# Optimization experiments

Hardware: AMD Instinct MI355X
Metric: run time of the kernel (lower is better)

## Reference

```python
import jax, jax.numpy as jnp
import numpy as np

N = 65536        # number of encoding vectors (flattened tokens)
K = 1024         # num_embeddings (codebook size)
D = 128          # embedding_dim
BETA = 0.25


def setup_inputs() -> dict:
    key = jax.random.key(0)
    k_enc, k_cb = jax.random.split(key)
    encoding = jax.random.normal(k_enc, (N, D), dtype=jnp.float32)
    # nn.Embedding weight initialized uniform(-1/K, 1/K)
    codebook = jax.random.uniform(k_cb, (K, D), dtype=jnp.float32,
                                  minval=-1.0 / K, maxval=1.0 / K)
    return {"encoding": encoding, "codebook": codebook}


def reference(encoding, codebook):
    # Nearest codebook entry per row. argmin of L2 distance == argmin of
    # squared distance; expand ||e - w||^2 = ||e||^2 - 2 e.w + ||w||^2.
    # ||e||^2 is constant per row, so it does not affect the argmin.
    scores = (-2.0 * jnp.einsum('nd,kd->nk', encoding, codebook)
              + jnp.sum(codebook * codebook, axis=-1)[None, :])  # [N, K]
    quantized_index = jnp.argmin(scores, axis=-1)                # [N] int
    quantized_embedding = codebook[quantized_index]              # [N, D] gather == onehot @ W

    sg = jax.lax.stop_gradient
    commitment_loss = jnp.mean((sg(quantized_embedding) - encoding) ** 2)
    embedding_loss = jnp.mean((quantized_embedding - sg(encoding)) ** 2)
    vq_loss = commitment_loss * BETA + embedding_loss

    # straight-through estimator
    quantized_st = encoding + sg(quantized_embedding - encoding)

    quantized_index = quantized_index[:, None]  # match torch unsqueeze(1) -> [N, 1]
    return (quantized_index, quantized_st, vq_loss, embedding_loss, commitment_loss)
```

## Files before the change

kernel.cpp:

```cpp
#include <hip/hip_runtime.h>


#define NROWS 65536
#define KCB   1024
#define DIM   128
#define DV    32
#define MSE_DENOM 8388608.0f
#define MARGIN 3.0e-5f
#define MARGINS 0.030720f
#define FLAGCAP 16384
#define CSCALE   1024.0f
#define CDESCALE 0.0009765625f

#define WS_CNORM_F  256
#define WS_CN1024_F 1280
#define WS_LIST_B   12288
#define WS_PH_B     77824
#define WS_NEEDED   339968

typedef __attribute__((ext_vector_type(16))) float float16v;
typedef _Float16 half8 __attribute__((ext_vector_type(8)));
union U4H8 { uint4 u; half8 h; };
union F4A  { float4 v; float f[4]; };
union F16V { float16v v; float f[16]; };
union HU   { _Float16 f; unsigned short u; };

__device__ __forceinline__ float fmed3(float a, float b, float c) {
  return __builtin_amdgcn_fmed3f(a, b, c);
}

__global__ __launch_bounds__(256) void vq_prep_pack(const float* __restrict__ C,
                                                    float* __restrict__ wsf,
                                                    uint4* __restrict__ PH) {
  const int b = blockIdx.x;
  if (b < 64) {
    int g = b * 256 + threadIdx.x;
    int mt = g >> 9, s = (g >> 6) & 7, l = g & 63;
    int cw = mt * 32 + (l & 31);
    int k0 = s * 16 + (l >> 5) * 8;
    const float* src = C + (size_t)cw * DIM + k0;
    float4 x0 = *(const float4*)src;
    float4 x1 = *(const float4*)(src + 4);
    unsigned h[8];
    {
      float v[8] = {x0.x, x0.y, x0.z, x0.w, x1.x, x1.y, x1.z, x1.w};
#pragma unroll
      for (int j = 0; j < 8; ++j) { HU u; u.f = (_Float16)(CSCALE * v[j]); h[j] = u.u; }
    }
    PH[g] = make_uint4(h[0] | (h[1] << 16), h[2] | (h[3] << 16),
                       h[4] | (h[5] << 16), h[6] | (h[7] << 16));
  } else {
    int k = (b - 64) * 256 + threadIdx.x;
    if (k == 0) { wsf[0] = 0.0f; ((unsigned*)wsf)[1] = 0u; }
    const float4* c4 = (const float4*)C + (size_t)k * DV;
    float s = 0.f;
#pragma unroll 8
    for (int i = 0; i < DV; ++i) {
      float4 v = c4[i];
      s = fmaf(v.x, v.x, s); s = fmaf(v.y, v.y, s);
      s = fmaf(v.z, v.z, s); s = fmaf(v.w, v.w, s);
    }
    wsf[WS_CNORM_F + k]  = s;
    wsf[WS_CN1024_F + k] = s * CSCALE;
  }
}

__global__ __launch_bounds__(256, 2) void vq_main11(const float* __restrict__ E,
                                                    const float* __restrict__ C,
                                                    float* __restrict__ wsf,
                                                    float* __restrict__ out) {
  __shared__ int BI[128];

  const int tid  = threadIdx.x;
  const int w    = tid >> 6;
  const int l    = tid & 63;
  const int half = l >> 5;
  const int rr   = l & 31;
  const int row0 = blockIdx.x * 128;
  const int row  = row0 + w * 32 + rr;

  const uint4*  PHg = (const uint4*)((const char*)wsf + WS_PH_B);
  const float4* CNb = (const float4*)(wsf + WS_CN1024_F);

  half8 beh[8];
  float s2 = 0.f;
  const float* erow = E + (size_t)row * DIM + half * 8;
#pragma unroll
  for (int s = 0; s < 8; ++s) {
    float4 x0 = *(const float4*)(erow + s * 16);
    float4 x1 = *(const float4*)(erow + s * 16 + 4);
    float v[8] = {x0.x, x0.y, x0.z, x0.w, x1.x, x1.y, x1.z, x1.w};
#pragma unroll
    for (int j = 0; j < 8; ++j) {
      float y = v[j];
      s2 = fmaf(y, y, s2);
      beh[s][j] = (_Float16)(-2.f * y);
    }
  }

  float m1 = 3.0e38f, m2 = 3.0e38f;
  int   bi = 0;

#pragma unroll 4
  for (int tg = 0; tg < 32; ++tg) {
    const uint4* src = PHg + (size_t)tg * 512 + l;
    U4H8 h0, h1, h2, h3, h4, h5, h6, h7;
    h0.u = src[0];   h1.u = src[64];  h2.u = src[128]; h3.u = src[192];
    h4.u = src[256]; h5.u = src[320]; h6.u = src[384]; h7.u = src[448];

    const float4* cn = CNb + tg * 8 + half;
    F4A c0, c1, c2, c3;
    c0.v = cn[0]; c1.v = cn[2]; c2.v = cn[4]; c3.v = cn[6];

    F16V accA, accB;
    accA.f[0]  = c0.f[0]; accA.f[1]  = c0.f[1]; accA.f[2]  = c0.f[2]; accA.f[3]  = c0.f[3];
    accA.f[4]  = c1.f[0]; accA.f[5]  = c1.f[1]; accA.f[6]  = c1.f[2]; accA.f[7]  = c1.f[3];
    accA.f[8]  = c2.f[0]; accA.f[9]  = c2.f[1]; accA.f[10] = c2.f[2]; accA.f[11] = c2.f[3];
    accA.f[12] = c3.f[0]; accA.f[13] = c3.f[1]; accA.f[14] = c3.f[2]; accA.f[15] = c3.f[3];
    accB.v = (float16v){0,0,0,0,0,0,0,0,0,0,0,0,0,0,0,0};

    accA.v = __builtin_amdgcn_mfma_f32_32x32x16_f16(h0.h, beh[0], accA.v, 0, 0, 0);
    accB.v = __builtin_amdgcn_mfma_f32_32x32x16_f16(h1.h, beh[1], accB.v, 0, 0, 0);
    accA.v = __builtin_amdgcn_mfma_f32_32x32x16_f16(h2.h, beh[2], accA.v, 0, 0, 0);
    accB.v = __builtin_amdgcn_mfma_f32_32x32x16_f16(h3.h, beh[3], accB.v, 0, 0, 0);
    accA.v = __builtin_amdgcn_mfma_f32_32x32x16_f16(h4.h, beh[4], accA.v, 0, 0, 0);
    accB.v = __builtin_amdgcn_mfma_f32_32x32x16_f16(h5.h, beh[5], accB.v, 0, 0, 0);
    accA.v = __builtin_amdgcn_mfma_f32_32x32x16_f16(h6.h, beh[6], accA.v, 0, 0, 0);
    accB.v = __builtin_amdgcn_mfma_f32_32x32x16_f16(h7.h, beh[7], accB.v, 0, 0, 0);

    const int kb = tg * 32 + half * 4;
#pragma unroll
    for (int reg = 0; reg < 16; ++reg) {
      float sc = accA.f[reg] + accB.f[reg];
      bool nb_ = sc < m1;
      m2 = fmed3(sc, m1, m2);
      m1 = fminf(sc, m1);
      bi = nb_ ? (kb + (reg >> 2) * 8 + (reg & 3)) : bi;
    }
  }

  {
    float om1 = __shfl_xor(m1, 32, 64);
    float om2 = __shfl_xor(m2, 32, 64);
    int   obi = __shfl_xor(bi, 32, 64);
    float nsv = fminf(fminf(m2, om2), fmaxf(m1, om1));
    if (om1 < m1 || (om1 == m1 && obi < bi)) { m1 = om1; bi = obi; }
    m2 = nsv;
  }
  float en = s2 + __shfl_xor(s2, 32, 64);

  if (half == 0) {
    const int r = w * 32 + rr;
    out[row] = (float)bi;
    BI[r] = bi;
    if (m2 - m1 < MARGINS) {
      unsigned idx = atomicAdd((unsigned*)wsf + 1, 1u);
      if (idx < FLAGCAP) ((int*)((char*)wsf + WS_LIST_B))[idx] = row;
    }
    float term = fmaf(m1, CDESCALE, en);
#pragma unroll
    for (int off = 16; off > 0; off >>= 1) term += __shfl_down(term, off);
    if (rr == 0) atomicAdd(wsf, term);
  }
  __syncthreads();

  const float4* C4   = (const float4*)C;
  float4*       out4 = (float4*)out;
#pragma unroll
  for (int it = 0; it < 16; ++it) {
    int flat = it * 256 + tid;
    int r = flat >> 5, d4 = flat & 31;
    out4[(NROWS / 4) + (size_t)(row0 + r) * DV + d4] = C4[(size_t)BI[r] * DV + d4];
  }
}

__global__ __launch_bounds__(256) void vq_fix(const float* __restrict__ E,
                                              const float* __restrict__ C,
                                              float* __restrict__ wsf,
                                              float* __restrict__ out) {
  __shared__ float4 eL[4][32];
  __shared__ float  RV[4][4];
  __shared__ int    RI[4][4];
  __shared__ int    RESi[4];
  const int tid = threadIdx.x;
  const int wv  = tid >> 6;
  const int ln  = tid & 63;

  if (blockIdx.x == 0 && tid == 0) {
    float mse = wsf[0] / MSE_DENOM;
    out[NROWS + NROWS * DIM + 0] = 1.25f * mse;
    out[NROWS + NROWS * DIM + 1] = mse;
    out[NROWS + NROWS * DIM + 2] = mse;
  }

  const int* list = (const int*)((const char*)wsf + WS_LIST_B);
  int nf = (int)((const unsigned*)wsf)[1];
  if (nf > FLAGCAP) nf = FLAGCAP;
  const float4* E4 = (const float4*)E;
  const float4* C4 = (const float4*)C;
  const float*  cn = wsf + WS_CNORM_F;
  float4* out4 = (float4*)out;

  for (int g = blockIdx.x; g * 4 < nf; g += gridDim.x) {
    const int base = g * 4;
    if (tid < 128) {
      int r = tid >> 5, d4 = tid & 31;
      int R = (base + r < nf) ? list[base + r] : list[base];
      eL[r][d4] = E4[(size_t)R * DV + d4];
    }
    __syncthreads();
    float bv[4] = {3.0e38f, 3.0e38f, 3.0e38f, 3.0e38f};
    int   bi[4] = {0, 0, 0, 0};
#pragma unroll
    for (int j = 0; j < 4; ++j) {
      int k = j * 256 + tid;
      float d0 = 0.f, d1 = 0.f, d2 = 0.f, d3 = 0.f;
#pragma unroll 4
      for (int d4 = 0; d4 < 32; ++d4) {
        float4 c = C4[(size_t)k * DV + d4];
        float4 e0 = eL[0][d4], e1 = eL[1][d4], e2 = eL[2][d4], e3 = eL[3][d4];
        d0 = fmaf(c.x, e0.x, d0); d0 = fmaf(c.y, e0.y, d0);
        d0 = fmaf(c.z, e0.z, d0); d0 = fmaf(c.w, e0.w, d0);
        d1 = fmaf(c.x, e1.x, d1); d1 = fmaf(c.y, e1.y, d1);
        d1 = fmaf(c.z, e1.z, d1); d1 = fmaf(c.w, e1.w, d1);
        d2 = fmaf(c.x, e2.x, d2); d2 = fmaf(c.y, e2.y, d2);
        d2 = fmaf(c.z, e2.z, d2); d2 = fmaf(c.w, e2.w, d2);
        d3 = fmaf(c.x, e3.x, d3); d3 = fmaf(c.y, e3.y, d3);
        d3 = fmaf(c.z, e3.z, d3); d3 = fmaf(c.w, e3.w, d3);
      }
      float cnk = cn[k];
      float s0 = fmaf(-2.f, d0, cnk);
      float s1 = fmaf(-2.f, d1, cnk);
      float s2 = fmaf(-2.f, d2, cnk);
      float s3 = fmaf(-2.f, d3, cnk);
      if (s0 < bv[0] || (s0 == bv[0] && k < bi[0])) { bv[0] = s0; bi[0] = k; }
      if (s1 < bv[1] || (s1 == bv[1] && k < bi[1])) { bv[1] = s1; bi[1] = k; }
      if (s2 < bv[2] || (s2 == bv[2] && k < bi[2])) { bv[2] = s2; bi[2] = k; }
      if (s3 < bv[3] || (s3 == bv[3] && k < bi[3])) { bv[3] = s3; bi[3] = k; }
    }
#pragma unroll
    for (int off = 32; off > 0; off >>= 1) {
#pragma unroll
      for (int r = 0; r < 4; ++r) {
        float wv_ = __shfl_down(bv[r], off);
        int   ji  = __shfl_down(bi[r], off);
        if (wv_ < bv[r] || (wv_ == bv[r] && ji < bi[r])) { bv[r] = wv_; bi[r] = ji; }
      }
    }
    if (ln == 0) {
#pragma unroll
      for (int r = 0; r < 4; ++r) { RV[wv][r] = bv[r]; RI[wv][r] = bi[r]; }
    }
    __syncthreads();
    if (tid < 4) {
      float v = RV[0][tid]; int i = RI[0][tid];
#pragma unroll
      for (int q = 1; q < 4; ++q) {
        float vv = RV[q][tid]; int ii = RI[q][tid];
        if (vv < v || (vv == v && ii < i)) { v = vv; i = ii; }
      }
      RESi[tid] = i;
      if (base + tid < nf) out[list[base + tid]] = (float)i;
    }
    __syncthreads();
    if (tid < 128) {
      int r = tid >> 5, d4 = tid & 31;
      if (base + r < nf) {
        int R = list[base + r];
        out4[(NROWS / 4) + (size_t)R * DV + d4] = C4[(size_t)RESi[r] * DV + d4];
      }
    }
    __syncthreads();
  }
}

__global__ __launch_bounds__(256) void vq_prep_fb(const float* __restrict__ C,
                                                  float* __restrict__ ws) {
  int k = blockIdx.x * 256 + threadIdx.x;
  if (k == 0) ws[0] = 0.0f;
  const float4* c4 = (const float4*)C + (size_t)k * DV;
  float s = 0.f;
#pragma unroll 8
  for (int i = 0; i < DV; ++i) {
    float4 v = c4[i];
    s = fmaf(v.x, v.x, s); s = fmaf(v.y, v.y, s);
    s = fmaf(v.z, v.z, s); s = fmaf(v.w, v.w, s);
  }
  ws[64 + k] = s;
}

__global__ __launch_bounds__(256) void vq_main_fb(const float* __restrict__ E,
                                                  const float* __restrict__ C,
                                                  const float* __restrict__ cnorm,
                                                  float* __restrict__ out,
                                                  float* __restrict__ lossacc) {
  __shared__ float smem[16384];
  float4* EsV = (float4*)smem;
  float4* CsV = (float4*)(smem + 8192);
  const int tid  = threadIdx.x;
  const int row0 = blockIdx.x * 64;
#pragma unroll
  for (int i = 0; i < 8; ++i) {
    int flat = i * 256 + tid;
    int r = flat >> 5, d4 = flat & 31;
    EsV[r * 32 + (d4 ^ (r & 31))] = ((const float4*)E)[(size_t)(row0 + r) * DV + d4];
  }
  const int tx = tid & 15, ty = tid >> 4;
  int rbase[4], rmask[4];
#pragma unroll
  for (int i = 0; i < 4; ++i) { int r = i * 16 + ty; rbase[i] = r * 32; rmask[i] = r & 31; }
  float bestv[4]; int besti[4];
#pragma unroll
  for (int i = 0; i < 4; ++i) { bestv[i] = 3.0e38f; besti[i] = 0; }
  for (int ch = 0; ch < 16; ++ch) {
    const int k0 = ch * 64;
    __syncthreads();
#pragma unroll
    for (int i = 0; i < 8; ++i) {
      int flat = i * 256 + tid;
      int k = flat >> 5, d4 = flat & 31;
      CsV[k * 32 + (d4 ^ (k & 31))] = ((const float4*)C)[(size_t)(k0 + k) * DV + d4];
    }
    __syncthreads();
    float acc[4][4] = {};
#pragma unroll 8
    for (int d4 = 0; d4 < DV; ++d4) {
      float4 a[4], b[4];
#pragma unroll
      for (int i = 0; i < 4; ++i) a[i] = EsV[rbase[i] + (d4 ^ rmask[i])];
#pragma unroll
      for (int j = 0; j < 4; ++j) { int k = j * 16 + tx; b[j] = CsV[k * 32 + (d4 ^ (k & 31))]; }
#pragma unroll
      for (int i = 0; i < 4; ++i)
#pragma unroll
        for (int j = 0; j < 4; ++j) {
          acc[i][j] = fmaf(a[i].x, b[j].x, acc[i][j]);
          acc[i][j] = fmaf(a[i].y, b[j].y, acc[i][j]);
          acc[i][j] = fmaf(a[i].z, b[j].z, acc[i][j]);
          acc[i][j] = fmaf(a[i].w, b[j].w, acc[i][j]);
        }
    }
#pragma unroll
    for (int j = 0; j < 4; ++j) {
      int kg = k0 + j * 16 + tx;
      float cnv = cnorm[kg];
#pragma unroll
      for (int i = 0; i < 4; ++i) {
        float s = fmaf(-2.0f, acc[i][j], cnv);
        if (s < bestv[i] || (s == bestv[i] && kg < besti[i])) { bestv[i] = s; besti[i] = kg; }
      }
    }
  }
  float* Rv = smem + 8192;
  int*   Ri = (int*)(smem + 9216);
  int*   BIf = (int*)(smem + 10240);
  __syncthreads();
#pragma unroll
  for (int i = 0; i < 4; ++i) {
    int r = i * 16 + ty;
    Rv[r * 16 + tx] = bestv[i];
    Ri[r * 16 + tx] = besti[i];
  }
  __syncthreads();
  if (tid < 64) {
    const int r = tid;
    float bv = Rv[r * 16]; int bi = Ri[r * 16];
#pragma unroll
    for (int t = 1; t < 16; ++t) {
      float v = Rv[r * 16 + t]; int ii = Ri[r * 16 + t];
      if (v < bv || (v == bv && ii < bi)) { bv = v; bi = ii; }
    }
    float en = 0.f;
#pragma unroll 8
    for (int d4 = 0; d4 < DV; ++d4) {
      float4 v = EsV[r * 32 + (d4 ^ (r & 31))];
      en = fmaf(v.x, v.x, en); en = fmaf(v.y, v.y, en);
      en = fmaf(v.z, v.z, en); en = fmaf(v.w, v.w, en);
    }
    out[row0 + r] = (float)bi;
    BIf[r] = bi;
    float blocksum = en + bv;
#pragma unroll
    for (int off = 32; off > 0; off >>= 1) blocksum += __shfl_down(blocksum, off);
    if (tid == 0) atomicAdd(lossacc, blocksum);
  }
  __syncthreads();
  const float4* C4   = (const float4*)C;
  float4*       out4 = (float4*)out;
  for (int flat = tid; flat < 64 * DV; flat += 256) {
    int r = flat >> 5, d4 = flat & 31;
    out4[(NROWS / 4) + (size_t)(row0 + r) * DV + d4] = C4[(size_t)BIf[r] * DV + d4];
  }
}

__global__ void vq_final_fb(const float* __restrict__ ws, float* __restrict__ out) {
  if (threadIdx.x == 0 && blockIdx.x == 0) {
    float mse = ws[0] / MSE_DENOM;
    out[NROWS + NROWS * DIM + 0] = 1.25f * mse;
    out[NROWS + NROWS * DIM + 1] = mse;
    out[NROWS + NROWS * DIM + 2] = mse;
  }
}

extern "C" void kernel_launch(void* const* d_in, const int* in_sizes, int n_in,
                              void* d_out, int out_size, void* d_ws, size_t ws_size,
                              hipStream_t stream) {
  const float* E = (const float*)d_in[0];
  const float* C = (const float*)d_in[1];
  float* out = (float*)d_out;
  float* wsf = (float*)d_ws;

  if (ws_size >= (size_t)WS_NEEDED) {
    uint4* PH = (uint4*)((char*)d_ws + WS_PH_B);
    vq_prep_pack<<<68, 256, 0, stream>>>(C, wsf, PH);
    vq_main11<<<NROWS / 128, 256, 0, stream>>>(E, C, wsf, out);
    vq_fix<<<512, 256, 0, stream>>>(E, C, wsf, out);
  } else {
    vq_prep_fb<<<4, 256, 0, stream>>>(C, wsf);
    vq_main_fb<<<NROWS / 64, 256, 0, stream>>>(E, C, wsf + 64, out, wsf);
    vq_final_fb<<<1, 64, 0, stream>>>(wsf, out);
  }
}
```

Before: 165.2 us.

## Split codebook across waves per 32-row block and merge top-2 via LDS

Each block now handles 32 rows instead of 128, and its four waves each scan a quarter of the codebook (8 tiles) for the same rows rather than all 32 tiles for separate rows. Per-wave best/second-best scores and indices are merged through shared memory before writing outputs and flagging near-ties. Occupancy is raised (launch bounds 5) and the two accumulators are collapsed into a single chained MFMA accumulator to cut registers. This trades a longer dependent MFMA chain, an extra barrier and 4x more blocks, each redundantly loading and converting the E rows in every wave, for shorter per-wave loops and more waves in flight.

```diff
diff --git a/kernel.cpp b/kernel.cpp
--- a/kernel.cpp
+++ b/kernel.cpp
@@ -65,19 +65,22 @@
   }
 }
 
-__global__ __launch_bounds__(256, 2) void vq_main11(const float* __restrict__ E,
+__global__ __launch_bounds__(256, 5) void vq_main12(const float* __restrict__ E,
                                                     const float* __restrict__ C,
                                                     float* __restrict__ wsf,
                                                     float* __restrict__ out) {
-  __shared__ int BI[128];
+  __shared__ float XM1[4][32];
+  __shared__ float XM2[4][32];
+  __shared__ int   XBI[4][32];
+  __shared__ int   BI[32];
 
   const int tid  = threadIdx.x;
   const int w    = tid >> 6;
   const int l    = tid & 63;
   const int half = l >> 5;
   const int rr   = l & 31;
-  const int row0 = blockIdx.x * 128;
-  const int row  = row0 + w * 32 + rr;
+  const int row0 = blockIdx.x * 32;
+  const int row  = row0 + rr;
 
   const uint4*  PHg = (const uint4*)((const char*)wsf + WS_PH_B);
   const float4* CNb = (const float4*)(wsf + WS_CN1024_F);
@@ -101,37 +104,41 @@
   float m1 = 3.0e38f, m2 = 3.0e38f;
   int   bi = 0;
 
-#pragma unroll 4
-  for (int tg = 0; tg < 32; ++tg) {
+#pragma unroll 2
+  for (int t = 0; t < 8; ++t) {
+    const int tg = w * 8 + t;
     const uint4* src = PHg + (size_t)tg * 512 + l;
-    U4H8 h0, h1, h2, h3, h4, h5, h6, h7;
-    h0.u = src[0];   h1.u = src[64];  h2.u = src[128]; h3.u = src[192];
-    h4.u = src[256]; h5.u = src[320]; h6.u = src[384]; h7.u = src[448];
 
     const float4* cn = CNb + tg * 8 + half;
     F4A c0, c1, c2, c3;
     c0.v = cn[0]; c1.v = cn[2]; c2.v = cn[4]; c3.v = cn[6];
-
-    F16V accA, accB;
-    accA.f[0]  = c0.f[0]; accA.f[1]  = c0.f[1]; accA.f[2]  = c0.f[2]; accA.f[3]  = c0.f[3];
-    accA.f[4]  = c1.f[0]; accA.f[5]  = c1.f[1]; accA.f[6]  = c1.f[2]; accA.f[7]  = c1.f[3];
-    accA.f[8]  = c2.f[0]; accA.f[9]  = c2.f[1]; accA.f[10] = c2.f[2]; accA.f[11] = c2.f[3];
-    accA.f[12] = c3.f[0]; accA.f[13] = c3.f[1]; accA.f[14] = c3.f[2]; accA.f[15] = c3.f[3];
-    accB.v = (float16v){0,0,0,0,0,0,0,0,0,0,0,0,0,0,0,0};
-
-    accA.v = __builtin_amdgcn_mfma_f32_32x32x16_f16(h0.h, beh[0], accA.v, 0, 0, 0);
-    accB.v = __builtin_amdgcn_mfma_f32_32x32x16_f16(h1.h, beh[1], accB.v, 0, 0, 0);
-    accA.v = __builtin_amdgcn_mfma_f32_32x32x16_f16(h2.h, beh[2], accA.v, 0, 0, 0);
-    accB.v = __builtin_amdgcn_mfma_f32_32x32x16_f16(h3.h, beh[3], accB.v, 0, 0, 0);
-    accA.v = __builtin_amdgcn_mfma_f32_32x32x16_f16(h4.h, beh[4], accA.v, 0, 0, 0);
-    accB.v = __builtin_amdgcn_mfma_f32_32x32x16_f16(h5.h, beh[5], accB.v, 0, 0, 0);
-    accA.v = __builtin_amdgcn_mfma_f32_32x32x16_f16(h6.h, beh[6], accA.v, 0, 0, 0);
-    accB.v = __builtin_amdgcn_mfma_f32_32x32x16_f16(h7.h, beh[7], accB.v, 0, 0, 0);
+    F16V acc;
+    acc.f[0]  = c0.f[0]; acc.f[1]  = c0.f[1]; acc.f[2]  = c0.f[2]; acc.f[3]  = c0.f[3];
+    acc.f[4]  = c1.f[0]; acc.f[5]  = c1.f[1]; acc.f[6]  = c1.f[2]; acc.f[7]  = c1.f[3];
+    acc.f[8]  = c2.f[0]; acc.f[9]  = c2.f[1]; acc.f[10] = c2.f[2]; acc.f[11] = c2.f[3];
+    acc.f[12] = c3.f[0]; acc.f[13] = c3.f[1]; acc.f[14] = c3.f[2]; acc.f[15] = c3.f[3];
+
+    {
+      U4H8 h0, h1, h2, h3;
+      h0.u = src[0];   h1.u = src[64];  h2.u = src[128]; h3.u = src[192];
+      acc.v = __builtin_amdgcn_mfma_f32_32x32x16_f16(h0.h, beh[0], acc.v, 0, 0, 0);
+      acc.v = __builtin_amdgcn_mfma_f32_32x32x16_f16(h1.h, beh[1], acc.v, 0, 0, 0);
+      acc.v = __builtin_amdgcn_mfma_f32_32x32x16_f16(h2.h, beh[2], acc.v, 0, 0, 0);
+      acc.v = __builtin_amdgcn_mfma_f32_32x32x16_f16(h3.h, beh[3], acc.v, 0, 0, 0);
+    }
+    {
+      U4H8 h4, h5, h6, h7;
+      h4.u = src[256]; h5.u = src[320]; h6.u = src[384]; h7.u = src[448];
+      acc.v = __builtin_amdgcn_mfma_f32_32x32x16_f16(h4.h, beh[4], acc.v, 0, 0, 0);
+      acc.v = __builtin_amdgcn_mfma_f32_32x32x16_f16(h5.h, beh[5], acc.v, 0, 0, 0);
+      acc.v = __builtin_amdgcn_mfma_f32_32x32x16_f16(h6.h, beh[6], acc.v, 0, 0, 0);
+      acc.v = __builtin_amdgcn_mfma_f32_32x32x16_f16(h7.h, beh[7], acc.v, 0, 0, 0);
+    }
 
     const int kb = tg * 32 + half * 4;
 #pragma unroll
     for (int reg = 0; reg < 16; ++reg) {
-      float sc = accA.f[reg] + accB.f[reg];
+      float sc = acc.f[reg];
       bool nb_ = sc < m1;
       m2 = fmed3(sc, m1, m2);
       m1 = fminf(sc, m1);
@@ -149,15 +156,26 @@
   }
   float en = s2 + __shfl_xor(s2, 32, 64);
 
-  if (half == 0) {
-    const int r = w * 32 + rr;
-    out[row] = (float)bi;
-    BI[r] = bi;
-    if (m2 - m1 < MARGINS) {
+  if (half == 0) { XM1[w][rr] = m1; XM2[w][rr] = m2; XBI[w][rr] = bi; }
+  __syncthreads();
+
+  if (w == 0 && half == 0) {
+    float b1 = XM1[0][rr], b2 = XM2[0][rr];
+    int   bb = XBI[0][rr];
+#pragma unroll
+    for (int q = 1; q < 4; ++q) {
+      float x1 = XM1[q][rr], x2 = XM2[q][rr];
+      int   xi = XBI[q][rr];
+      b2 = fminf(fminf(b2, x2), fmaxf(b1, x1));
+      if (x1 < b1 || (x1 == b1 && xi < bb)) { b1 = x1; bb = xi; }
+    }
+    out[row] = (float)bb;
+    BI[rr] = bb;
+    if (b2 - b1 < MARGINS) {
       unsigned idx = atomicAdd((unsigned*)wsf + 1, 1u);
       if (idx < FLAGCAP) ((int*)((char*)wsf + WS_LIST_B))[idx] = row;
     }
-    float term = fmaf(m1, CDESCALE, en);
+    float term = fmaf(b1, CDESCALE, en);
 #pragma unroll
     for (int off = 16; off > 0; off >>= 1) term += __shfl_down(term, off);
     if (rr == 0) atomicAdd(wsf, term);
@@ -167,7 +185,7 @@
   const float4* C4   = (const float4*)C;
   float4*       out4 = (float4*)out;
 #pragma unroll
-  for (int it = 0; it < 16; ++it) {
+  for (int it = 0; it < 4; ++it) {
     int flat = it * 256 + tid;
     int r = flat >> 5, d4 = flat & 31;
     out4[(NROWS / 4) + (size_t)(row0 + r) * DV + d4] = C4[(size_t)BI[r] * DV + d4];
@@ -413,7 +431,7 @@
   if (ws_size >= (size_t)WS_NEEDED) {
     uint4* PH = (uint4*)((char*)d_ws + WS_PH_B);
     vq_prep_pack<<<68, 256, 0, stream>>>(C, wsf, PH);
-    vq_main11<<<NROWS / 128, 256, 0, stream>>>(E, C, wsf, out);
+    vq_main12<<<NROWS / 32, 256, 0, stream>>>(E, C, wsf, out);
     vq_fix<<<512, 256, 0, stream>>>(E, C, wsf, out);
   } else {
     vq_prep_fb<<<4, 256, 0, stream>>>(C, wsf);
```

Result: slower. 181.6 us (+9.9%).
